# Performance work log

Measured on AMD Instinct MI355X. Metric: run time of the kernel, lower is better.

The kernel has to match this reference:

```python
import math
import jax, jax.numpy as jnp
import numpy as np

KERNEL_SIZE = 3
H_VAL = 0.35


def _dt_kernel(dtype):
    # kornia: meshgrid coords shifted by -floor(k/2), kernel = exp(hypot(x,y) / -h)
    k, h = KERNEL_SIZE, H_VAL
    r = k // 2
    ys, xs = jnp.meshgrid(jnp.arange(k, dtype=dtype) - r,
                          jnp.arange(k, dtype=dtype) - r, indexing='ij')
    return jnp.exp(jnp.hypot(xs, ys) / -h)[None, None]  # [1,1,k,k] (OIHW)


def _conv_replicate(x, kernel):
    # filter2d with border_type='replicate': edge-pad then VALID conv.
    # Kernel is symmetric, so correlation == convolution.
    pad = KERNEL_SIZE // 2
    xp = jnp.pad(x, ((0, 0), (0, 0), (pad, pad), (pad, pad)), mode='edge')
    return jax.lax.conv_general_dilated(
        xp, kernel, window_strides=(1, 1), padding='VALID',
        dimension_numbers=('NCHW', 'OIHW', 'NCHW'))


def setup_inputs() -> dict:
    key = jax.random.key(0)
    B, C, H, W = 8, 3, 160, 160
    u = jax.random.uniform(key, (B, C, H, W), dtype=jnp.float32)
    image = (u < 0.001).astype(jnp.float32)  # sparse binary seed mask
    return {"image": image}


def reference(image):
    k, h = KERNEL_SIZE, H_VAL
    B, C, H, W = image.shape
    n_iters = math.ceil(max(H, W) / (k // 2))  # static: depends only on shape
    kernel = _dt_kernel(image.dtype)
    x = image.reshape(B * C, 1, H, W)  # module merges channels into batch

    def body(i, carry):
        out, boundary = carry
        u = _conv_replicate(boundary, kernel)
        # cdt = nan_to_num(-h*log(u), posinf=0): u==0 -> +inf -> 0; safe-log form
        cdt = jnp.where(u > 0, -h * jnp.log(jnp.where(u > 0, u, 1.0)), 0.0)
        mask = (cdt > 0).astype(image.dtype)
        offset = jnp.floor_divide(i * k, 2).astype(image.dtype)  # i*kernel_size//2
        out = out + (offset + cdt) * mask
        boundary = jnp.where(mask == 1, jnp.ones_like(boundary), boundary)
        return (out, boundary)

    # Fixed trip count (torch early-exits on mask.sum()==0, but extra iterations
    # are no-ops once the mask is empty, so running all n_iters is equivalent).
    out, _ = jax.lax.fori_loop(0, n_iters, body, (jnp.zeros_like(x), x))
    return out.reshape(B, C, H, W)
```

## Files before the change

### kernel.cpp

```cpp
#include <hip/hip_runtime.h>


#define DT_W 160
#define DT_H 160
#define DT_NPIX (DT_W * DT_H)
#define MAXS 256
#define TILE 32
#define TW 34
#define NH (TW * TW)
#define HVAL 0.35f
#define TPB 256
#define CPT 5
#define LOADS (DT_NPIX / 4 / TPB)

__global__ __launch_bounds__(TPB) void dt_fused(const float* __restrict__ img,
                                                float* __restrict__ out) {
  __shared__ int slds[MAXS];
  __shared__ int cnt;
  __shared__ unsigned char dlds[NH];

  const int tx0 = blockIdx.x * TILE;
  const int ty0 = blockIdx.y * TILE;
  const int imgIdx = blockIdx.z;
  const int tid = threadIdx.x;
  float* o = out + imgIdx * DT_NPIX;

  const float4* im4 = (const float4*)(img + imgIdx * DT_NPIX);
  float4 vv[LOADS];
#pragma unroll
  for (int k = 0; k < LOADS; ++k) vv[k] = im4[tid + k * TPB];
  __builtin_amdgcn_sched_barrier(0);

  if (tid == 0) cnt = 0;
  __syncthreads();

#pragma unroll
  for (int k = 0; k < LOADS; ++k) {
    const float4 v = vv[k];
    if (fmaxf(fmaxf(v.x, v.y), fmaxf(v.z, v.w)) > 0.0f) {
      const float c4[4] = {v.x, v.y, v.z, v.w};
      const int base = (tid + k * TPB) * 4;
#pragma unroll
      for (int j = 0; j < 4; ++j) {
        if (c4[j] > 0.0f) {
          const int i = atomicAdd(&cnt, 1);
          if (i < MAXS) {
            const int p = base + j;
            const int y = p / DT_W, x = p - y * DT_W;
            slds[i] = x | (y << 16);
          }
        }
      }
    }
  }
  __syncthreads();
  const int n = cnt < MAXS ? cnt : MAXS;

  const int pix0 = tid * 4;
  const int py = pix0 >> 5, px0 = pix0 & 31;
  float* const orow = &o[(ty0 + py) * DT_W + tx0 + px0];

  if (n == 0) {
    *(float4*)orow = make_float4(0.f, 0.f, 0.f, 0.f);
    return;
  }

  int gx[CPT], gy[CPT], dmin[CPT];
#pragma unroll
  for (int k = 0; k < CPT; ++k) {
    int c = tid + k * TPB;
    if (c >= NH) c = NH - 1;
    const int hy = c / TW, hx = c - hy * TW;
    int x = tx0 - 1 + hx;
    gx[k] = x < 0 ? 0 : (x > DT_W - 1 ? DT_W - 1 : x);
    int y = ty0 - 1 + hy;
    gy[k] = y < 0 ? 0 : (y > DT_H - 1 ? DT_H - 1 : y);
    dmin[k] = 0x7ffffff;
  }

  const int myseed = slds[tid & 63];
  const int n64 = n < 64 ? n : 64;
  for (int s = 0; s < n64; ++s) {
    const int sv = __builtin_amdgcn_readlane(myseed, s);
    const int sx = sv & 0xffff, sy = sv >> 16;
#pragma unroll
    for (int k = 0; k < CPT; ++k) {
      const int dx = abs(gx[k] - sx), dy = abs(gy[k] - sy);
      const int dd = dx > dy ? dx : dy;
      dmin[k] = dd < dmin[k] ? dd : dmin[k];
    }
  }
  for (int s = 64; s < n; ++s) {
    const int sv = slds[s];
    const int sx = sv & 0xffff, sy = sv >> 16;
#pragma unroll
    for (int k = 0; k < CPT; ++k) {
      const int dx = abs(gx[k] - sx), dy = abs(gy[k] - sy);
      const int dd = dx > dy ? dx : dy;
      dmin[k] = dd < dmin[k] ? dd : dmin[k];
    }
  }
#pragma unroll
  for (int k = 0; k < CPT; ++k) {
    const int c = tid + k * TPB;
    if (c < NH) dlds[c] = (unsigned char)dmin[k];
  }
  __syncthreads();

  const float w1 = expf(-1.0f / HVAL);
  const float w2 = expf(-1.41421356237309515f / HVAL);
  const int hx0 = px0 + 1, hy = py + 1;
  unsigned char r0[6], r1[6], r2[6];
#pragma unroll
  for (int c = 0; c < 6; ++c) {
    r0[c] = dlds[(hy - 1) * TW + hx0 - 1 + c];
    r1[c] = dlds[hy * TW + hx0 - 1 + c];
    r2[c] = dlds[(hy + 1) * TW + hx0 - 1 + c];
  }
  float res[4];
#pragma unroll
  for (int i = 0; i < 4; ++i) {
    const int d = r1[i + 1];
    float val = 0.0f;
    if (d > 0) {
      const int t = d - 1;
      const int ns = (r1[i] == t) + (r1[i + 2] == t) +
                     (r0[i + 1] == t) + (r2[i + 1] == t);
      const int nd = (r0[i] == t) + (r0[i + 2] == t) +
                     (r2[i] == t) + (r2[i + 2] == t);
      const float u = w1 * (float)ns + w2 * (float)nd;
      val = (float)((t * 3) >> 1) - HVAL * __logf(u);
    }
    res[i] = val;
  }
  *(float4*)orow = make_float4(res[0], res[1], res[2], res[3]);
}

extern "C" void kernel_launch(void* const* d_in, const int* in_sizes, int n_in,
                              void* d_out, int out_size, void* d_ws,
                              size_t ws_size, hipStream_t stream) {
  const float* img = (const float*)d_in[0];
  float* out = (float*)d_out;
  const int n_img = in_sizes[0] / DT_NPIX;
  dim3 grid(DT_W / TILE, DT_H / TILE, n_img);
  dt_fused<<<grid, TPB, 0, stream>>>(img, out);
}
```

Before: 18.96 us.

## Double block size, pack distance search into short2 SIMD, re-read seed pixels

Raises threads per block to 512 so each thread handles 2 halo distance cells in the seed scan and 2 output pixels. The Chebyshev min-distance loop now runs on packed 16-bit short2 vectors, with the aim of using packed integer ops to halve per-seed ALU work. The image scan keeps only a per-thread bitmask of nonzero float4s instead of holding all loads in registers, and reloads the flagged float4s later. This lowers register pressure at the cost of a second global read for the few nonzero chunks, and each block now does a larger redundant full-image scan split across more threads.

Measured after the change: 18.03 us. 4.9% less time.

```diff
diff --git a/kernel.cpp b/kernel.cpp
--- a/kernel.cpp
+++ b/kernel.cpp
@@ -9,9 +9,11 @@
 #define TW 34
 #define NH (TW * TW)
 #define HVAL 0.35f
-#define TPB 256
-#define CPT 5
-#define LOADS (DT_NPIX / 4 / TPB)
+#define TPB 512
+#define NF4 (DT_NPIX / 4)
+#define LOADS_FULL (NF4 / TPB)
+
+typedef short short2v __attribute__((ext_vector_type(2)));
 
 __global__ __launch_bounds__(TPB) void dt_fused(const float* __restrict__ img,
                                                 float* __restrict__ out) {
@@ -21,33 +23,40 @@
 
   const int tx0 = blockIdx.x * TILE;
   const int ty0 = blockIdx.y * TILE;
-  const int imgIdx = blockIdx.z;
   const int tid = threadIdx.x;
-  float* o = out + imgIdx * DT_NPIX;
+  float* o = out + blockIdx.z * DT_NPIX;
+  const float4* im4 = (const float4*)(img + blockIdx.z * DT_NPIX);
 
-  const float4* im4 = (const float4*)(img + imgIdx * DT_NPIX);
-  float4 vv[LOADS];
+  unsigned pmask = 0;
 #pragma unroll
-  for (int k = 0; k < LOADS; ++k) vv[k] = im4[tid + k * TPB];
-  __builtin_amdgcn_sched_barrier(0);
-
+  for (int k = 0; k < LOADS_FULL; ++k) {
+    const float4 v = im4[tid + k * TPB];
+    if (v.x > 0.f || v.y > 0.f || v.z > 0.f || v.w > 0.f) pmask |= (1u << k);
+  }
+  if (tid < NF4 - LOADS_FULL * TPB) {
+    const float4 v = im4[tid + LOADS_FULL * TPB];
+    if (v.x > 0.f || v.y > 0.f || v.z > 0.f || v.w > 0.f)
+      pmask |= (1u << LOADS_FULL);
+  }
   if (tid == 0) cnt = 0;
   __syncthreads();
 
+  if (pmask) {
 #pragma unroll
-  for (int k = 0; k < LOADS; ++k) {
-    const float4 v = vv[k];
-    if (fmaxf(fmaxf(v.x, v.y), fmaxf(v.z, v.w)) > 0.0f) {
-      const float c4[4] = {v.x, v.y, v.z, v.w};
-      const int base = (tid + k * TPB) * 4;
+    for (int k = 0; k <= LOADS_FULL; ++k) {
+      if (pmask & (1u << k)) {
+        const int i4 = tid + k * TPB;
+        const float4 v = im4[i4];
+        const float c4[4] = {v.x, v.y, v.z, v.w};
 #pragma unroll
-      for (int j = 0; j < 4; ++j) {
-        if (c4[j] > 0.0f) {
-          const int i = atomicAdd(&cnt, 1);
-          if (i < MAXS) {
-            const int p = base + j;
-            const int y = p / DT_W, x = p - y * DT_W;
-            slds[i] = x | (y << 16);
+        for (int j = 0; j < 4; ++j) {
+          if (c4[j] > 0.f) {
+            const int i = atomicAdd(&cnt, 1);
+            if (i < MAXS) {
+              const int p = i4 * 4 + j;
+              const int y = p / DT_W, x = p - y * DT_W;
+              slds[i] = x | (y << 16);
+            }
           }
         }
       }
@@ -56,70 +65,85 @@
   __syncthreads();
   const int n = cnt < MAXS ? cnt : MAXS;
 
-  const int pix0 = tid * 4;
+  const int pix0 = tid * 2;
   const int py = pix0 >> 5, px0 = pix0 & 31;
   float* const orow = &o[(ty0 + py) * DT_W + tx0 + px0];
 
   if (n == 0) {
-    *(float4*)orow = make_float4(0.f, 0.f, 0.f, 0.f);
+    *(float2*)orow = make_float2(0.f, 0.f);
     return;
   }
 
-  int gx[CPT], gy[CPT], dmin[CPT];
+  short2v gxA, gyA, gxB, gyB;
+  {
+    int cs[2] = {2 * tid, 1024 + 2 * tid};
+    short gx2[4], gy2[4];
 #pragma unroll
-  for (int k = 0; k < CPT; ++k) {
-    int c = tid + k * TPB;
-    if (c >= NH) c = NH - 1;
-    const int hy = c / TW, hx = c - hy * TW;
-    int x = tx0 - 1 + hx;
-    gx[k] = x < 0 ? 0 : (x > DT_W - 1 ? DT_W - 1 : x);
-    int y = ty0 - 1 + hy;
-    gy[k] = y < 0 ? 0 : (y > DT_H - 1 ? DT_H - 1 : y);
-    dmin[k] = 0x7ffffff;
+    for (int pi = 0; pi < 2; ++pi) {
+#pragma unroll
+      for (int j = 0; j < 2; ++j) {
+        int c = cs[pi] + j;
+        if (c >= NH) c = NH - 1;
+        const int hy = c / TW, hx = c - hy * TW;
+        int x = tx0 - 1 + hx;
+        x = x < 0 ? 0 : (x > DT_W - 1 ? DT_W - 1 : x);
+        int y = ty0 - 1 + hy;
+        y = y < 0 ? 0 : (y > DT_H - 1 ? DT_H - 1 : y);
+        gx2[pi * 2 + j] = (short)x;
+        gy2[pi * 2 + j] = (short)y;
+      }
+    }
+    gxA.x = gx2[0]; gxA.y = gx2[1]; gxB.x = gx2[2]; gxB.y = gx2[3];
+    gyA.x = gy2[0]; gyA.y = gy2[1]; gyB.x = gy2[2]; gyB.y = gy2[3];
   }
+
+  short2v dminA, dminB;
+  dminA.x = 511; dminA.y = 511; dminB.x = 511; dminB.y = 511;
+
+  auto upd = [&](int sv) {
+    const short sx = (short)(sv & 0xffff), sy = (short)(sv >> 16);
+    short2v sx2, sy2;
+    sx2.x = sx; sx2.y = sx; sy2.x = sy; sy2.y = sy;
+    const short2v ddA =
+        __builtin_elementwise_max(__builtin_elementwise_abs((short2v)(gxA - sx2)),
+                                  __builtin_elementwise_abs((short2v)(gyA - sy2)));
+    const short2v ddB =
+        __builtin_elementwise_max(__builtin_elementwise_abs((short2v)(gxB - sx2)),
+                                  __builtin_elementwise_abs((short2v)(gyB - sy2)));
+    dminA = __builtin_elementwise_min(dminA, ddA);
+    dminB = __builtin_elementwise_min(dminB, ddB);
+  };
 
   const int myseed = slds[tid & 63];
   const int n64 = n < 64 ? n : 64;
-  for (int s = 0; s < n64; ++s) {
-    const int sv = __builtin_amdgcn_readlane(myseed, s);
-    const int sx = sv & 0xffff, sy = sv >> 16;
-#pragma unroll
-    for (int k = 0; k < CPT; ++k) {
-      const int dx = abs(gx[k] - sx), dy = abs(gy[k] - sy);
-      const int dd = dx > dy ? dx : dy;
-      dmin[k] = dd < dmin[k] ? dd : dmin[k];
-    }
-  }
-  for (int s = 64; s < n; ++s) {
-    const int sv = slds[s];
-    const int sx = sv & 0xffff, sy = sv >> 16;
-#pragma unroll
-    for (int k = 0; k < CPT; ++k) {
-      const int dx = abs(gx[k] - sx), dy = abs(gy[k] - sy);
-      const int dd = dx > dy ? dx : dy;
-      dmin[k] = dd < dmin[k] ? dd : dmin[k];
-    }
-  }
-#pragma unroll
-  for (int k = 0; k < CPT; ++k) {
-    const int c = tid + k * TPB;
-    if (c < NH) dlds[c] = (unsigned char)dmin[k];
+  for (int s = 0; s < n64; ++s)
+    upd(__builtin_amdgcn_readlane(myseed, s));
+  for (int s = 64; s < n; ++s)
+    upd(slds[s]);
+
+  {
+    *(unsigned short*)&dlds[2 * tid] =
+        (unsigned short)((dminA.x & 0xff) | ((dminA.y & 0xff) << 8));
+    const int c = 1024 + 2 * tid;
+    if (c < NH)
+      *(unsigned short*)&dlds[c] =
+          (unsigned short)((dminB.x & 0xff) | ((dminB.y & 0xff) << 8));
   }
   __syncthreads();
 
   const float w1 = expf(-1.0f / HVAL);
   const float w2 = expf(-1.41421356237309515f / HVAL);
   const int hx0 = px0 + 1, hy = py + 1;
-  unsigned char r0[6], r1[6], r2[6];
+  unsigned char r0[4], r1[4], r2[4];
 #pragma unroll
-  for (int c = 0; c < 6; ++c) {
+  for (int c = 0; c < 4; ++c) {
     r0[c] = dlds[(hy - 1) * TW + hx0 - 1 + c];
     r1[c] = dlds[hy * TW + hx0 - 1 + c];
     r2[c] = dlds[(hy + 1) * TW + hx0 - 1 + c];
   }
-  float res[4];
+  float res[2];
 #pragma unroll
-  for (int i = 0; i < 4; ++i) {
+  for (int i = 0; i < 2; ++i) {
     const int d = r1[i + 1];
     float val = 0.0f;
     if (d > 0) {
@@ -133,7 +157,7 @@
     }
     res[i] = val;
   }
-  *(float4*)orow = make_float4(res[0], res[1], res[2], res[3]);
+  *(float2*)orow = make_float2(res[0], res[1]);
 }
 
 extern "C" void kernel_launch(void* const* d_in, const int* in_sizes, int n_in,
```

## Split seed extraction into separate kernel and pack distance math into short2

Applied to the files above, without the earlier changes.

Seed extraction moves out of the fused kernel into its own pass that runs once per image and writes the seed lists and counts to workspace. Before, every one of the 25 tiles rescanned the whole 160x160 image. The main kernel reads the precomputed seeds and does the Chebyshev min-distance search with packed 16-bit vector ops, so each thread handles two halo pixels per instruction. This adds a second kernel launch and a global-memory round trip, and it relies on workspace layout (counts at offset 0, seeds at offset 32). It also assumes at most 32 images.

Result: faster. 17.79 us (-6.2%).

```diff
diff --git a/kernel.cpp b/kernel.cpp
--- a/kernel.cpp
+++ b/kernel.cpp
@@ -4,50 +4,39 @@
 #define DT_W 160
 #define DT_H 160
 #define DT_NPIX (DT_W * DT_H)
+#define NF4 (DT_NPIX / 4)
 #define MAXS 256
 #define TILE 32
 #define TW 34
 #define NH (TW * TW)
 #define HVAL 0.35f
-#define TPB 256
-#define CPT 5
-#define LOADS (DT_NPIX / 4 / TPB)
+#define SENTINEL 0x7fff7fff
+#define K1_TPB 1024
+#define K2_TPB 256
 
-__global__ __launch_bounds__(TPB) void dt_fused(const float* __restrict__ img,
-                                                float* __restrict__ out) {
-  __shared__ int slds[MAXS];
+typedef short short2v __attribute__((ext_vector_type(2)));
+
+__global__ __launch_bounds__(K1_TPB) void dt_seeds(const float* __restrict__ img,
+                                                   int* __restrict__ cnts,
+                                                   int* __restrict__ seeds) {
   __shared__ int cnt;
-  __shared__ unsigned char dlds[NH];
-
-  const int tx0 = blockIdx.x * TILE;
-  const int ty0 = blockIdx.y * TILE;
-  const int imgIdx = blockIdx.z;
-  const int tid = threadIdx.x;
-  float* o = out + imgIdx * DT_NPIX;
-
-  const float4* im4 = (const float4*)(img + imgIdx * DT_NPIX);
-  float4 vv[LOADS];
-#pragma unroll
-  for (int k = 0; k < LOADS; ++k) vv[k] = im4[tid + k * TPB];
-  __builtin_amdgcn_sched_barrier(0);
-
+  __shared__ int sl[MAXS];
+  const int imgIdx = blockIdx.x, tid = threadIdx.x;
   if (tid == 0) cnt = 0;
   __syncthreads();
-
-#pragma unroll
-  for (int k = 0; k < LOADS; ++k) {
-    const float4 v = vv[k];
-    if (fmaxf(fmaxf(v.x, v.y), fmaxf(v.z, v.w)) > 0.0f) {
+  const float4* im4 = (const float4*)(img + imgIdx * DT_NPIX);
+  for (int i4 = tid; i4 < NF4; i4 += K1_TPB) {
+    const float4 v = im4[i4];
+    if (v.x > 0.f || v.y > 0.f || v.z > 0.f || v.w > 0.f) {
       const float c4[4] = {v.x, v.y, v.z, v.w};
-      const int base = (tid + k * TPB) * 4;
 #pragma unroll
       for (int j = 0; j < 4; ++j) {
-        if (c4[j] > 0.0f) {
+        if (c4[j] > 0.f) {
           const int i = atomicAdd(&cnt, 1);
           if (i < MAXS) {
-            const int p = base + j;
-            const int y = p / DT_W, x = p - y * DT_W;
-            slds[i] = x | (y << 16);
+            const int p = i4 * 4 + j;
+            const int y = p / DT_W;
+            sl[i] = (p - y * DT_W) | (y << 16);
           }
         }
       }
@@ -55,6 +44,24 @@
   }
   __syncthreads();
   const int n = cnt < MAXS ? cnt : MAXS;
+  if (tid == 0) cnts[imgIdx] = n;
+  int* sg = seeds + imgIdx * MAXS;
+  for (int i = tid; i < n; i += K1_TPB) sg[i] = sl[i];
+  for (int i = n + tid; i < 64; i += K1_TPB) sg[i] = SENTINEL;
+}
+
+__global__ __launch_bounds__(K2_TPB) void dt_main(const int* __restrict__ cnts,
+                                                  const int* __restrict__ seeds,
+                                                  float* __restrict__ out) {
+  __shared__ unsigned char dlds[NH];
+  const int tx0 = blockIdx.x * TILE;
+  const int ty0 = blockIdx.y * TILE;
+  const int z = blockIdx.z;
+  const int tid = threadIdx.x;
+  float* o = out + z * DT_NPIX;
+
+  const int n = cnts[z];
+  const int myseed = seeds[z * MAXS + (tid & 63)];
 
   const int pix0 = tid * 4;
   const int py = pix0 >> 5, px0 = pix0 & 31;
@@ -65,45 +72,49 @@
     return;
   }
 
-  int gx[CPT], gy[CPT], dmin[CPT];
+  short2v gx[3], gy[3], dmin[3];
 #pragma unroll
-  for (int k = 0; k < CPT; ++k) {
-    int c = tid + k * TPB;
-    if (c >= NH) c = NH - 1;
-    const int hy = c / TW, hx = c - hy * TW;
-    int x = tx0 - 1 + hx;
-    gx[k] = x < 0 ? 0 : (x > DT_W - 1 ? DT_W - 1 : x);
-    int y = ty0 - 1 + hy;
-    gy[k] = y < 0 ? 0 : (y > DT_H - 1 ? DT_H - 1 : y);
-    dmin[k] = 0x7ffffff;
+  for (int b = 0; b < 3; ++b) {
+#pragma unroll
+    for (int j = 0; j < 2; ++j) {
+      int c = b * 512 + 2 * tid + j;
+      if (c >= NH) c = NH - 1;
+      const int hy = c / TW, hx = c - hy * TW;
+      int x = tx0 - 1 + hx;
+      x = x < 0 ? 0 : (x > DT_W - 1 ? DT_W - 1 : x);
+      int y = ty0 - 1 + hy;
+      y = y < 0 ? 0 : (y > DT_H - 1 ? DT_H - 1 : y);
+      gx[b][j] = (short)x;
+      gy[b][j] = (short)y;
+    }
+    dmin[b][0] = 511; dmin[b][1] = 511;
   }
 
-  const int myseed = slds[tid & 63];
+  auto upd = [&](int sv) {
+    const short sx = (short)(sv & 0xffff), sy = (short)(sv >> 16);
+    short2v sx2, sy2;
+    sx2[0] = sx; sx2[1] = sx; sy2[0] = sy; sy2[1] = sy;
+#pragma unroll
+    for (int b = 0; b < 3; ++b) {
+      const short2v dd = __builtin_elementwise_max(
+          __builtin_elementwise_abs((short2v)(gx[b] - sx2)),
+          __builtin_elementwise_abs((short2v)(gy[b] - sy2)));
+      dmin[b] = __builtin_elementwise_min(dmin[b], dd);
+    }
+  };
+
   const int n64 = n < 64 ? n : 64;
-  for (int s = 0; s < n64; ++s) {
-    const int sv = __builtin_amdgcn_readlane(myseed, s);
-    const int sx = sv & 0xffff, sy = sv >> 16;
+  for (int s = 0; s < n64; ++s)
+    upd(__builtin_amdgcn_readlane(myseed, s));
+  for (int s = 64; s < n; ++s)
+    upd(seeds[z * MAXS + s]);
+
 #pragma unroll
-    for (int k = 0; k < CPT; ++k) {
-      const int dx = abs(gx[k] - sx), dy = abs(gy[k] - sy);
-      const int dd = dx > dy ? dx : dy;
-      dmin[k] = dd < dmin[k] ? dd : dmin[k];
-    }
-  }
-  for (int s = 64; s < n; ++s) {
-    const int sv = slds[s];
-    const int sx = sv & 0xffff, sy = sv >> 16;
-#pragma unroll
-    for (int k = 0; k < CPT; ++k) {
-      const int dx = abs(gx[k] - sx), dy = abs(gy[k] - sy);
-      const int dd = dx > dy ? dx : dy;
-      dmin[k] = dd < dmin[k] ? dd : dmin[k];
-    }
-  }
-#pragma unroll
-  for (int k = 0; k < CPT; ++k) {
-    const int c = tid + k * TPB;
-    if (c < NH) dlds[c] = (unsigned char)dmin[k];
+  for (int b = 0; b < 3; ++b) {
+    const int c = b * 512 + 2 * tid;
+    if (c < NH)
+      *(unsigned short*)&dlds[c] =
+          (unsigned short)((dmin[b][0] & 0xff) | ((dmin[b][1] & 0xff) << 8));
   }
   __syncthreads();
 
@@ -142,6 +153,11 @@
   const float* img = (const float*)d_in[0];
   float* out = (float*)d_out;
   const int n_img = in_sizes[0] / DT_NPIX;
+
+  int* cnts = (int*)d_ws;
+  int* seeds = (int*)d_ws + 32;
+
+  dt_seeds<<<n_img, K1_TPB, 0, stream>>>(img, cnts, seeds);
   dim3 grid(DT_W / TILE, DT_H / TILE, n_img);
-  dt_fused<<<grid, TPB, 0, stream>>>(img, out);
+  dt_main<<<grid, K2_TPB, 0, stream>>>(cnts, seeds, out);
 }
```
